# Kernel optimization log

Measured on AMD Instinct MI355X. Metric: run time of the kernel, lower is better.

The kernel has to match this reference:

```python
import jax, jax.numpy as jnp
import numpy as np

B, L, D_IN, D_H, N_CLS = 512, 256, 300, 96, 20
N = B * L            # total nodes = 131072
DEG = 8
E = N * DEG          # 1,048,576 edges
VOCAB = 50001        # num_words + 1 (padding row)
STEP = 2
NEG_SLOPE = 0.2


def setup_inputs() -> dict:
    key = jax.random.key(0)
    ks = jax.random.split(key, 24)
    node_ids = jax.random.randint(ks[0], (N,), 0, 50000)
    # block-local edges: each edge stays within its graph's node range
    gid = jnp.repeat(jnp.arange(B), L * DEG)           # [E]
    src = gid * L + jax.random.randint(ks[1], (E,), 0, L)
    dst = gid * L + jax.random.randint(ks[2], (E,), 0, L)

    def xavier(k, shape):
        fan_in, fan_out = shape[0], shape[-1]
        a = float(np.sqrt(6.0 / (fan_in + fan_out)))
        return jax.random.uniform(k, shape, jnp.float32, -a, a)

    inp = {
        "node_ids": node_ids, "src": src, "dst": dst,
        "embed": jax.random.normal(ks[3], (VOCAB, D_IN), jnp.float32),
        "We": xavier(ks[4], (D_IN, D_H)), "be": jnp.zeros((D_H,), jnp.float32),
        "Wg": xavier(ks[5], (D_H, D_H)),
        "att_src": xavier(ks[6], (D_H,)), "att_dst": xavier(ks[7], (D_H,)),
        "bg": jnp.zeros((D_H,), jnp.float32),
        "Wz0": xavier(ks[8], (D_H, D_H)), "bz0": jnp.zeros((D_H,), jnp.float32),
        "Wz1": xavier(ks[9], (D_H, D_H)), "bz1": jnp.zeros((D_H,), jnp.float32),
        "Wr0": xavier(ks[10], (D_H, D_H)), "br0": jnp.zeros((D_H,), jnp.float32),
        "Wr1": xavier(ks[11], (D_H, D_H)), "br1": jnp.zeros((D_H,), jnp.float32),
        "Wh0": xavier(ks[12], (D_H, D_H)), "bh0": jnp.zeros((D_H,), jnp.float32),
        "Wh1": xavier(ks[13], (D_H, D_H)), "bh1": jnp.zeros((D_H,), jnp.float32),
        "Wemb": xavier(ks[14], (D_H, D_H)),
        "Wmlp": xavier(ks[15], (D_H, N_CLS)),
    }
    return inp


def _forward(node_ids, src, dst, embed, We, be, Wg, att_src, att_dst, bg,
             Wz0, bz0, Wz1, bz1, Wr0, br0, Wr1, br1, Wh0, bh0, Wh1, bh1,
             Wemb, Wmlp):
    # embedding lookup + encode (dropout off, eval)
    x = embed[node_ids]                                  # [N, D_IN]
    x = jnp.tanh(x @ We + be)                            # [N, D_H]

    # self loops (GATConv add_self_loops=True, heads=1)
    loop = jnp.arange(N)
    s = jnp.concatenate([src, loop])
    d = jnp.concatenate([dst, loop])

    for _ in range(STEP):
        # ---- GATConv ----
        h = x @ Wg                                       # [N, D_H]
        a_s = h @ att_src                                # [N]
        a_d = h @ att_dst                                # [N]
        e = a_s[s] + a_d[d]
        e = jnp.where(e > 0, e, NEG_SLOPE * e)           # leaky_relu
        # segment softmax over incoming edges of each target node
        m = jax.ops.segment_max(e, d, num_segments=N)
        ex = jnp.exp(e - m[d])
        denom = jax.ops.segment_sum(ex, d, num_segments=N)
        alpha = ex / denom[d]                            # [E+N]
        a = jax.ops.segment_sum(alpha[:, None] * h[s], d, num_segments=N) + bg
        # ---- GRU update (act=tanh) ----
        z = jax.nn.sigmoid(a @ Wz0 + bz0 + x @ Wz1 + bz1)
        r = jax.nn.sigmoid(a @ Wr0 + br0 + x @ Wr1 + br1)
        hh = jnp.tanh(a @ Wh0 + bh0 + (x * r) @ Wh1 + bh1)
        x = hh * z + x * (1.0 - z)

    # graph2batch: equal-length graphs -> reshape, mask is all ones
    xb = x.reshape(B, L, D_H)
    y = jnp.tanh(xb @ Wemb)                              # [B, L, D_H]
    pooled = y.max(axis=1) + y.mean(axis=1)              # max + mean readout
    return pooled @ Wmlp                                 # [B, N_CLS]


def reference(node_ids, src, dst, embed, We, be, Wg, att_src, att_dst, bg,
              Wz0, bz0, Wz1, bz1, Wr0, br0, Wr1, br1, Wh0, bh0, Wh1, bh1,
              Wemb, Wmlp):
    return _forward(node_ids, src, dst, embed, We, be, Wg, att_src, att_dst, bg,
                    Wz0, bz0, Wz1, bz1, Wr0, br0, Wr1, br1, Wh0, bh0, Wh1, bh1,
                    Wemb, Wmlp)
```

## Files before the change

### kernel.cpp

```cpp
#include <hip/hip_runtime.h>
#include <hip/hip_bf16.h>

#define NNODES 131072
#define LGRAPH 256
#define BGRAPH 512
#define DIN 300
#define DH 96
#define EPG 2048
#define VOCAB 50001
#define NCLS 20
#define NEG 0.2f
#define EMB_ROWS 50048
#define EMB_K 320
#define WS 100
#define XS 104

typedef __attribute__((ext_vector_type(4))) float f32x4;
typedef __attribute__((ext_vector_type(8))) short bf16x8;
typedef __attribute__((ext_vector_type(8))) unsigned short u16x8;
#define MFMA16(a, b, c) __builtin_amdgcn_mfma_f32_16x16x32_bf16(a, b, c, 0, 0, 0)

__device__ __forceinline__ unsigned short f2b(float f) {
  __hip_bfloat16 h = __float2bfloat16(f);
  return *reinterpret_cast<unsigned short*>(&h);
}
__device__ __forceinline__ float b2f(unsigned short u) {
  unsigned v = ((unsigned)u) << 16;
  return __uint_as_float(v);
}
__device__ __forceinline__ float sigm(float v) { return 1.f / (1.f + __expf(-v)); }
__device__ __forceinline__ float ftanh(float x) {
  float ax = fabsf(x);
  float e = __expf(ax + ax);
  float t = 1.f - 2.f / (e + 1.f);
  return copysignf(t, x);
}

__global__ void k_prep_w(const float* __restrict__ Wg, const float* __restrict__ Wz0,
                         const float* __restrict__ Wz1, const float* __restrict__ Wr0,
                         const float* __restrict__ Wr1, const float* __restrict__ Wh0,
                         const float* __restrict__ Wh1, const float* __restrict__ Wemb,
                         const float* __restrict__ We,
                         const float* __restrict__ bz0, const float* __restrict__ bz1,
                         const float* __restrict__ br0, const float* __restrict__ br1,
                         const float* __restrict__ bh0, const float* __restrict__ bh1,
                         unsigned short* __restrict__ WT, unsigned short* __restrict__ WeT,
                         float* __restrict__ bc) {
  const int b = blockIdx.x, t = threadIdx.x;
  if (b < 8) {
    const float* src = (b == 0) ? Wg : (b == 1) ? Wz0 : (b == 2) ? Wz1 : (b == 3) ? Wr0
                     : (b == 4) ? Wr1 : (b == 5) ? Wh0 : (b == 6) ? Wh1 : Wemb;
    unsigned short* dst = WT + b * DH * DH;
    for (int i = t; i < DH * DH; i += 256) {
      int c = i / DH, k = i - c * DH;
      dst[i] = f2b(src[k * DH + c]);
    }
  } else if (b == 8) {
    for (int i = t; i < DH * EMB_K; i += 256) {
      int c = i / EMB_K, k = i - c * EMB_K;
      WeT[i] = (k < DIN) ? f2b(We[k * DH + c]) : (unsigned short)0;
    }
  } else {
    if (t < DH) {
      bc[t] = bz0[t] + bz1[t];
      bc[DH + t] = br0[t] + br1[t];
      bc[2 * DH + t] = bh0[t] + bh1[t];
    }
  }
}

__device__ __forceinline__ bf16x8 ldcvt(const float* __restrict__ p, int row, int ko) {
  bf16x8 r;
  if (row < VOCAB) {
    float4 c0 = (ko + 4 <= DIN) ? *(const float4*)&p[row * DIN + ko]
                                : make_float4(0.f, 0.f, 0.f, 0.f);
    float4 c1 = (ko + 8 <= DIN) ? *(const float4*)&p[row * DIN + ko + 4]
                                : make_float4(0.f, 0.f, 0.f, 0.f);
    r[0] = (short)f2b(c0.x); r[1] = (short)f2b(c0.y);
    r[2] = (short)f2b(c0.z); r[3] = (short)f2b(c0.w);
    r[4] = (short)f2b(c1.x); r[5] = (short)f2b(c1.y);
    r[6] = (short)f2b(c1.z); r[7] = (short)f2b(c1.w);
  } else {
    #pragma unroll
    for (int j = 0; j < 8; ++j) r[j] = 0;
  }
  return r;
}

__global__ void k_emb_mm(const float* __restrict__ embed,
                         const unsigned short* __restrict__ WeT,
                         unsigned short* __restrict__ Tb) {
  const int t = threadIdx.x, w = t >> 6, l = t & 63, li = l & 15, lh = l >> 4;
  const int wbase = blockIdx.x * 128 + w * 32;
  f32x4 acc[2][6];
  #pragma unroll
  for (int rt = 0; rt < 2; rt++)
    #pragma unroll
    for (int ct = 0; ct < 6; ct++) acc[rt][ct] = (f32x4)0.f;
  for (int ks = 0; ks < 10; ++ks) {
    const int ko = lh * 8 + ks * 32;
    bf16x8 aA0 = ldcvt(embed, wbase + li, ko);
    bf16x8 aA1 = ldcvt(embed, wbase + 16 + li, ko);
    #pragma unroll
    for (int ct = 0; ct < 6; ct++) {
      bf16x8 bB = *(const bf16x8*)&WeT[(ct * 16 + li) * EMB_K + ko];
      acc[0][ct] = MFMA16(aA0, bB, acc[0][ct]);
      acc[1][ct] = MFMA16(aA1, bB, acc[1][ct]);
    }
  }
  #pragma unroll
  for (int rt = 0; rt < 2; rt++)
    #pragma unroll
    for (int ct = 0; ct < 6; ct++)
      #pragma unroll
      for (int r = 0; r < 4; r++)
        Tb[(wbase + rt * 16 + lh * 4 + r) * DH + ct * 16 + li] = f2b(acc[rt][ct][r]);
}

__global__ void k_gather(const int* __restrict__ ids, const unsigned short* __restrict__ Tb,
                         const float* __restrict__ be, unsigned short* __restrict__ xb) {
  const int total = NNODES * (DH / 8);
  for (int i = blockIdx.x * blockDim.x + threadIdx.x; i < total;
       i += gridDim.x * blockDim.x) {
    int n = i / (DH / 8);
    int q = i - n * (DH / 8);
    u16x8 v = *(const u16x8*)&Tb[ids[n] * DH + q * 8];
    u16x8 o;
    #pragma unroll
    for (int j = 0; j < 8; ++j) o[j] = f2b(ftanh(b2f(v[j]) + be[q * 8 + j]));
    *(u16x8*)&xb[i * 8] = o;
  }
}

__global__ __launch_bounds__(256) void k_h(
    const unsigned short* __restrict__ xb, const unsigned short* __restrict__ WgT,
    const float* __restrict__ att_s, const float* __restrict__ att_d,
    unsigned short* __restrict__ h, float* __restrict__ a_s,
    float* __restrict__ a_d) {
  __shared__ __align__(16) unsigned short sW[DH * WS];
  const int t = threadIdx.x, w = t >> 6, l = t & 63, li = l & 15, lh = l >> 4;
  const int wbase = blockIdx.x * 128 + w * 32;
  for (int i = t; i < DH * 12; i += 256) {
    int r = i / 12, c8 = i - r * 12;
    *(int4*)&sW[r * WS + c8 * 8] = *(const int4*)&WgT[r * DH + c8 * 8];
  }
  __syncthreads();
  f32x4 acc[2][6];
  #pragma unroll
  for (int rt = 0; rt < 2; rt++)
    #pragma unroll
    for (int ct = 0; ct < 6; ct++) acc[rt][ct] = (f32x4)0.f;
  #pragma unroll
  for (int ks = 0; ks < 3; ++ks) {
    const int ko = lh * 8 + ks * 32;
    bf16x8 aA0 = *(const bf16x8*)&xb[(wbase + li) * DH + ko];
    bf16x8 aA1 = *(const bf16x8*)&xb[(wbase + 16 + li) * DH + ko];
    #pragma unroll
    for (int ct = 0; ct < 6; ct++) {
      bf16x8 bB = *(const bf16x8*)&sW[(ct * 16 + li) * WS + ko];
      acc[0][ct] = MFMA16(aA0, bB, acc[0][ct]);
      acc[1][ct] = MFMA16(aA1, bB, acc[1][ct]);
    }
  }
  float ps[2][4] = {}, pd[2][4] = {};
  #pragma unroll
  for (int rt = 0; rt < 2; rt++)
    #pragma unroll
    for (int ct = 0; ct < 6; ct++) {
      const int col = ct * 16 + li;
      const float as_ = att_s[col], ad_ = att_d[col];
      #pragma unroll
      for (int r = 0; r < 4; r++) {
        float v = acc[rt][ct][r];
        h[(wbase + rt * 16 + lh * 4 + r) * DH + col] = f2b(v);
        ps[rt][r] += v * as_;
        pd[rt][r] += v * ad_;
      }
    }
  #pragma unroll
  for (int rt = 0; rt < 2; rt++)
    #pragma unroll
    for (int r = 0; r < 4; r++) {
      float s = ps[rt][r], d = pd[rt][r];
      #pragma unroll
      for (int m = 1; m < 16; m <<= 1) { s += __shfl_xor(s, m); d += __shfl_xor(d, m); }
      if (li == 0) {
        const int row = wbase + rt * 16 + lh * 4 + r;
        a_s[row] = s;
        a_d[row] = d;
      }
    }
}

__global__ __launch_bounds__(512, 4) void k_att(
    const int* __restrict__ src, const int* __restrict__ dst,
    const unsigned short* __restrict__ h, const float* __restrict__ a_sg,
    const float* __restrict__ a_dg, const float* __restrict__ bg,
    unsigned short* __restrict__ aout) {
  __shared__ __align__(16) unsigned short sH[LGRAPH * XS];
  __shared__ float s_ev[EPG];
  __shared__ unsigned char s_sl[EPG], s_dl[EPG];
  __shared__ unsigned char s_srcS[EPG];
  __shared__ int s_cnt[LGRAPH], s_off[LGRAPH], s_pos[LGRAPH];
  __shared__ float s_as[LGRAPH], s_ad[LGRAPH];
  __shared__ float s_bg[DH];
  const int g = blockIdx.x, t = threadIdx.x;
  const int nb = g * LGRAPH;
  if (t < LGRAPH) { s_cnt[t] = 0; s_as[t] = a_sg[nb + t]; s_ad[t] = a_dg[nb + t]; }
  if (t < DH) s_bg[t] = bg[t];
  #pragma unroll
  for (int j = 0; j < 6; ++j) {
    int idx = t + 512 * j;
    int row = idx / 12, ch = idx - row * 12;
    *(int4*)&sH[row * XS + ch * 8] = *(const int4*)&h[(nb + row) * DH + ch * 8];
  }
  __syncthreads();
  for (int e = t; e < EPG; e += 512) {
    int sl = src[g * EPG + e] - nb, dl = dst[g * EPG + e] - nb;
    s_sl[e] = (unsigned char)sl;
    s_dl[e] = (unsigned char)dl;
    atomicAdd(&s_cnt[dl], 1);
  }
  __syncthreads();
  if (t < 64) {
    int carry = 0;
    #pragma unroll
    for (int c = 0; c < 4; ++c) {
      int v = s_cnt[c * 64 + t];
      int x = v;
      #pragma unroll
      for (int o = 1; o < 64; o <<= 1) {
        int y = __shfl_up(x, o);
        if (t >= o) x += y;
      }
      s_off[c * 64 + t] = x - v + carry;
      carry += __shfl(x, 63);
    }
  }
  __syncthreads();
  if (t < LGRAPH) s_pos[t] = s_off[t];
  __syncthreads();
  for (int e = t; e < EPG; e += 512) {
    int sl = s_sl[e], dl = s_dl[e];
    float ee = s_as[sl] + s_ad[dl];
    ee = ee > 0.f ? ee : NEG * ee;
    int pos = atomicAdd(&s_pos[dl], 1);
    s_srcS[pos] = (unsigned char)sl;
    s_ev[pos] = ee;
  }
  __syncthreads();
  {
    const int d = t >> 1, half = t & 1;
    const int beg = s_off[d], end = beg + s_cnt[d];
    float ss = s_as[d] + s_ad[d];
    ss = ss > 0.f ? ss : NEG * ss;
    float m = ss;
    for (int i = beg; i < end; ++i) m = fmaxf(m, s_ev[i]);
    const int cbase = half * 48;
    float acc[48];
    float wself = __expf(ss - m);
    float den = wself;
    #pragma unroll
    for (int k = 0; k < 6; ++k) {
      u16x8 v = *(const u16x8*)&sH[d * XS + cbase + k * 8];
      #pragma unroll
      for (int j = 0; j < 8; ++j) acc[k * 8 + j] = wself * b2f(v[j]);
    }
    for (int i = beg; i < end; ++i) {
      float wv = __expf(s_ev[i] - m);
      den += wv;
      int sl2 = s_srcS[i];
      #pragma unroll
      for (int k = 0; k < 6; ++k) {
        u16x8 v = *(const u16x8*)&sH[sl2 * XS + cbase + k * 8];
        #pragma unroll
        for (int j = 0; j < 8; ++j) acc[k * 8 + j] += wv * b2f(v[j]);
      }
    }
    float inv = 1.f / den;
    unsigned short* op = &aout[(nb + d) * DH + cbase];
    #pragma unroll
    for (int k = 0; k < 6; ++k) {
      u16x8 o;
      #pragma unroll
      for (int j = 0; j < 8; ++j) o[j] = f2b(acc[k * 8 + j] * inv + s_bg[cbase + k * 8 + j]);
      *(u16x8*)&op[k * 8] = o;
    }
  }
}

__global__ __launch_bounds__(512, 2) void k_gru(
    const unsigned short* __restrict__ ab, unsigned short* __restrict__ xb,
    const unsigned short* __restrict__ WT, const float* __restrict__ bc) {
  __shared__ __align__(16) unsigned short sW[6 * DH * WS];
  __shared__ __align__(16) unsigned short sX[128 * WS];
  const int t = threadIdx.x, w = t >> 6, l = t & 63, li = l & 15, lh = l >> 4;
  const int wr = w >> 1, wc = w & 1;
  #pragma unroll
  for (int m = 0; m < 6; ++m) {
    const int srcm = (m == 0) ? 3 : (m == 1) ? 4 : (m == 2) ? 1 : (m == 3) ? 2 : (m == 4) ? 5 : 6;
    const unsigned short* srcp = WT + srcm * DH * DH;
    for (int i = t; i < DH * 12; i += 512) {
      int r = i / 12, c8 = i - r * 12;
      *(int4*)&sW[(m * DH + r) * WS + c8 * 8] = *(const int4*)&srcp[r * DH + c8 * 8];
    }
  }
  float zb_[3], rb_[3], hb_[3];
  #pragma unroll
  for (int ct = 0; ct < 3; ++ct) {
    const int col = wc * 48 + ct * 16 + li;
    zb_[ct] = bc[col]; rb_[ct] = bc[DH + col]; hb_[ct] = bc[2 * DH + col];
  }

  for (int tile = 0; tile < 4; ++tile) {
    const int nb0 = (blockIdx.x * 4 + tile) * 128;
    __syncthreads();
    #pragma unroll
    for (int j = 0; j < 3; ++j) {
      int idx = t + 512 * j;
      int row = idx / 12, ch = idx - row * 12;
      *(int4*)&sX[row * WS + ch * 8] = *(const int4*)&xb[(nb0 + row) * DH + ch * 8];
    }
    __syncthreads();
    bf16x8 aA[2][3], aX[2][3];
    #pragma unroll
    for (int rt = 0; rt < 2; rt++)
      #pragma unroll
      for (int ks = 0; ks < 3; ks++) {
        const int row = wr * 32 + rt * 16 + li;
        const int ko = lh * 8 + ks * 32;
        aA[rt][ks] = *(const bf16x8*)&ab[(nb0 + row) * DH + ko];
        aX[rt][ks] = *(const bf16x8*)&sX[row * WS + ko];
      }
    float xo[2][3][4];
    #pragma unroll
    for (int rt = 0; rt < 2; rt++)
      #pragma unroll
      for (int ct = 0; ct < 3; ct++)
        #pragma unroll
        for (int r = 0; r < 4; r++)
          xo[rt][ct][r] = b2f(sX[(wr * 32 + rt * 16 + lh * 4 + r) * WS + wc * 48 + ct * 16 + li]);
    f32x4 accR[2][3], accZ[2][3];
    #pragma unroll
    for (int rt = 0; rt < 2; rt++)
      #pragma unroll
      for (int ct = 0; ct < 3; ct++) { accR[rt][ct] = (f32x4)0.f; accZ[rt][ct] = (f32x4)0.f; }
    #pragma unroll
    for (int ks = 0; ks < 3; ks++) {
      const int ko = lh * 8 + ks * 32;
      #pragma unroll
      for (int ct = 0; ct < 3; ct++) {
        const int wrow = wc * 48 + ct * 16 + li;
        bf16x8 w_r0 = *(const bf16x8*)&sW[(0 * DH + wrow) * WS + ko];
        bf16x8 w_r1 = *(const bf16x8*)&sW[(1 * DH + wrow) * WS + ko];
        bf16x8 w_z0 = *(const bf16x8*)&sW[(2 * DH + wrow) * WS + ko];
        bf16x8 w_z1 = *(const bf16x8*)&sW[(3 * DH + wrow) * WS + ko];
        #pragma unroll
        for (int rt = 0; rt < 2; rt++) {
          accR[rt][ct] = MFMA16(aA[rt][ks], w_r0, accR[rt][ct]);
          accR[rt][ct] = MFMA16(aX[rt][ks], w_r1, accR[rt][ct]);
          accZ[rt][ct] = MFMA16(aA[rt][ks], w_z0, accZ[rt][ct]);
          accZ[rt][ct] = MFMA16(aX[rt][ks], w_z1, accZ[rt][ct]);
        }
      }
    }
    __syncthreads();
    #pragma unroll
    for (int rt = 0; rt < 2; rt++)
      #pragma unroll
      for (int ct = 0; ct < 3; ct++) {
        const int col = wc * 48 + ct * 16 + li;
        #pragma unroll
        for (int r = 0; r < 4; r++) {
          float rv = sigm(accR[rt][ct][r] + rb_[ct]);
          sX[(wr * 32 + rt * 16 + lh * 4 + r) * WS + col] = f2b(xo[rt][ct][r] * rv);
        }
      }
    __syncthreads();
    bf16x8 aU[2][3];
    #pragma unroll
    for (int rt = 0; rt < 2; rt++)
      #pragma unroll
      for (int ks = 0; ks < 3; ks++)
        aU[rt][ks] = *(const bf16x8*)&sX[(wr * 32 + rt * 16 + li) * WS + lh * 8 + ks * 32];
    __syncthreads();
    f32x4 accH[2][3];
    #pragma unroll
    for (int rt = 0; rt < 2; rt++)
      #pragma unroll
      for (int ct = 0; ct < 3; ct++) accH[rt][ct] = (f32x4)0.f;
    #pragma unroll
    for (int ks = 0; ks < 3; ks++) {
      const int ko = lh * 8 + ks * 32;
      #pragma unroll
      for (int ct = 0; ct < 3; ct++) {
        const int wrow = wc * 48 + ct * 16 + li;
        bf16x8 w_h0 = *(const bf16x8*)&sW[(4 * DH + wrow) * WS + ko];
        bf16x8 w_h1 = *(const bf16x8*)&sW[(5 * DH + wrow) * WS + ko];
        #pragma unroll
        for (int rt = 0; rt < 2; rt++) {
          accH[rt][ct] = MFMA16(aA[rt][ks], w_h0, accH[rt][ct]);
          accH[rt][ct] = MFMA16(aU[rt][ks], w_h1, accH[rt][ct]);
        }
      }
    }
    #pragma unroll
    for (int rt = 0; rt < 2; rt++)
      #pragma unroll
      for (int ct = 0; ct < 3; ct++) {
        const int col = wc * 48 + ct * 16 + li;
        #pragma unroll
        for (int r = 0; r < 4; r++) {
          float z = sigm(accZ[rt][ct][r] + zb_[ct]);
          float hh = ftanh(accH[rt][ct][r] + hb_[ct]);
          float xn = hh * z + xo[rt][ct][r] * (1.f - z);
          sX[(wr * 32 + rt * 16 + lh * 4 + r) * WS + col] = f2b(xn);
        }
      }
    __syncthreads();
    #pragma unroll
    for (int j = 0; j < 3; ++j) {
      int idx = t + 512 * j;
      int row = idx / 12, ch = idx - row * 12;
      *(int4*)&xb[(nb0 + row) * DH + ch * 8] = *(const int4*)&sX[row * WS + ch * 8];
    }
  }
}

__global__ __launch_bounds__(256) void k_readout(
    const unsigned short* __restrict__ xb, const unsigned short* __restrict__ WembT,
    const float* __restrict__ Wmlp, float* __restrict__ out) {
  __shared__ __align__(16) unsigned short sW[DH * WS];
  __shared__ float pmaxs[4][DH], psums[4][DH];
  __shared__ float spool[DH];
  const int g = blockIdx.x, t = threadIdx.x, w = t >> 6, l = t & 63, li = l & 15, lh = l >> 4;
  const int wbase = g * LGRAPH + w * 64;
  for (int i = t; i < DH * 12; i += 256) {
    int r = i / 12, c8 = i - r * 12;
    *(int4*)&sW[r * WS + c8 * 8] = *(const int4*)&WembT[r * DH + c8 * 8];
  }
  __syncthreads();
  f32x4 acc[4][6];
  #pragma unroll
  for (int rt = 0; rt < 4; rt++)
    #pragma unroll
    for (int ct = 0; ct < 6; ct++) acc[rt][ct] = (f32x4)0.f;
  #pragma unroll
  for (int ks = 0; ks < 3; ks++) {
    const int ko = lh * 8 + ks * 32;
    bf16x8 aA[4];
    #pragma unroll
    for (int rt = 0; rt < 4; rt++)
      aA[rt] = *(const bf16x8*)&xb[(wbase + rt * 16 + li) * DH + ko];
    #pragma unroll
    for (int ct = 0; ct < 6; ct++) {
      bf16x8 bB = *(const bf16x8*)&sW[(ct * 16 + li) * WS + ko];
      #pragma unroll
      for (int rt = 0; rt < 4; rt++) acc[rt][ct] = MFMA16(aA[rt], bB, acc[rt][ct]);
    }
  }
  float pm[6], psu[6];
  #pragma unroll
  for (int ct = 0; ct < 6; ct++) {
    float mx = -1e30f, sm = 0.f;
    #pragma unroll
    for (int rt = 0; rt < 4; rt++)
      #pragma unroll
      for (int r = 0; r < 4; r++) {
        float y = ftanh(acc[rt][ct][r]);
        mx = fmaxf(mx, y);
        sm += y;
      }
    pm[ct] = mx; psu[ct] = sm;
  }
  #pragma unroll
  for (int ct = 0; ct < 6; ct++) {
    pm[ct] = fmaxf(pm[ct], __shfl_xor(pm[ct], 16));
    psu[ct] += __shfl_xor(psu[ct], 16);
    pm[ct] = fmaxf(pm[ct], __shfl_xor(pm[ct], 32));
    psu[ct] += __shfl_xor(psu[ct], 32);
  }
  if (lh == 0) {
    #pragma unroll
    for (int ct = 0; ct < 6; ct++) {
      pmaxs[w][ct * 16 + li] = pm[ct];
      psums[w][ct * 16 + li] = psu[ct];
    }
  }
  __syncthreads();
  if (t < DH) {
    float mx = fmaxf(fmaxf(pmaxs[0][t], pmaxs[1][t]), fmaxf(pmaxs[2][t], pmaxs[3][t]));
    float sm = psums[0][t] + psums[1][t] + psums[2][t] + psums[3][t];
    spool[t] = mx + sm * (1.f / LGRAPH);
  }
  __syncthreads();
  if (t < NCLS) {
    float a = 0.f;
    for (int k = 0; k < DH; ++k) a += spool[k] * Wmlp[k * NCLS + t];
    out[g * NCLS + t] = a;
  }
}

extern "C" void kernel_launch(void* const* d_in, const int* in_sizes, int n_in,
                              void* d_out, int out_size, void* d_ws, size_t ws_size,
                              hipStream_t stream) {
  const int*   node_ids = (const int*)d_in[0];
  const int*   src      = (const int*)d_in[1];
  const int*   dst      = (const int*)d_in[2];
  const float* embed    = (const float*)d_in[3];
  const float* We   = (const float*)d_in[4];
  const float* be   = (const float*)d_in[5];
  const float* Wg   = (const float*)d_in[6];
  const float* att_src = (const float*)d_in[7];
  const float* att_dst = (const float*)d_in[8];
  const float* bg   = (const float*)d_in[9];
  const float* Wz0  = (const float*)d_in[10];
  const float* bz0  = (const float*)d_in[11];
  const float* Wz1  = (const float*)d_in[12];
  const float* bz1  = (const float*)d_in[13];
  const float* Wr0  = (const float*)d_in[14];
  const float* br0  = (const float*)d_in[15];
  const float* Wr1  = (const float*)d_in[16];
  const float* br1  = (const float*)d_in[17];
  const float* Wh0  = (const float*)d_in[18];
  const float* bh0  = (const float*)d_in[19];
  const float* Wh1  = (const float*)d_in[20];
  const float* bh1  = (const float*)d_in[21];
  const float* Wemb = (const float*)d_in[22];
  const float* Wmlp = (const float*)d_in[23];
  float* out = (float*)d_out;

  char* w_ = (char*)d_ws;
  unsigned short* xb   = (unsigned short*)(w_ + 0);
  unsigned short* ab   = (unsigned short*)(w_ + 25165824);
  unsigned short* h    = (unsigned short*)(w_ + 50331648);
  unsigned short* Tb   = (unsigned short*)(w_ + 75497472);
  float*          a_s  = (float*)(w_ + 85106688);
  float*          a_d  = (float*)(w_ + 85630976);
  unsigned short* WT   = (unsigned short*)(w_ + 86155264);
  unsigned short* WeT  = (unsigned short*)(w_ + 86302720);
  float*          bc   = (float*)(w_ + 86364160);

  unsigned short* WgT  = WT + 0 * DH * DH;
  unsigned short* WembT= WT + 7 * DH * DH;

  hipLaunchKernelGGL(k_prep_w, dim3(10), dim3(256), 0, stream,
                     Wg, Wz0, Wz1, Wr0, Wr1, Wh0, Wh1, Wemb, We,
                     bz0, bz1, br0, br1, bh0, bh1, WT, WeT, bc);
  hipLaunchKernelGGL(k_emb_mm, dim3(EMB_ROWS / 128), dim3(256), 0, stream, embed, WeT, Tb);
  hipLaunchKernelGGL(k_gather, dim3(2048), dim3(256), 0, stream, node_ids, Tb, be, xb);
  for (int s = 0; s < 2; ++s) {
    hipLaunchKernelGGL(k_h, dim3(NNODES / 128), dim3(256), 0, stream,
                       xb, WgT, att_src, att_dst, h, a_s, a_d);
    hipLaunchKernelGGL(k_att, dim3(BGRAPH), dim3(512), 0, stream,
                       src, dst, h, a_s, a_d, bg, ab);
    hipLaunchKernelGGL(k_gru, dim3(256), dim3(512), 0, stream, ab, xb, WT, bc);
  }
  hipLaunchKernelGGL(k_readout, dim3(BGRAPH), dim3(256), 0, stream, xb, WembT, Wmlp, out);
}
```

Measured before the change: 246.0 us.

## Fuse embedding gather with first GAT projection and widen GRU to 12 waves

Merges the gather/tanh encode kernel with the first-step Wg projection and attention-score computation, so the encoded rows are consumed from shared memory instead of being re-read from global memory by a separate launch. The GRU kernel is also reorganised from 8 waves (4x2) to 12 waves (4x3) per block, each covering 32 output columns instead of 48, to reduce per-thread register use and add parallelism. The fused kernel holds the Wg fragments in registers, and the larger GRU block with launch bounds of 3 blocks per CU may be limited by LDS, since each block keeps all six weight matrices in shared memory.

```diff
diff --git a/kernel.cpp b/kernel.cpp
--- a/kernel.cpp
+++ b/kernel.cpp
@@ -117,19 +117,85 @@
         Tb[(wbase + rt * 16 + lh * 4 + r) * DH + ct * 16 + li] = f2b(acc[rt][ct][r]);
 }
 
-__global__ void k_gather(const int* __restrict__ ids, const unsigned short* __restrict__ Tb,
-                         const float* __restrict__ be, unsigned short* __restrict__ xb) {
-  const int total = NNODES * (DH / 8);
-  for (int i = blockIdx.x * blockDim.x + threadIdx.x; i < total;
-       i += gridDim.x * blockDim.x) {
-    int n = i / (DH / 8);
-    int q = i - n * (DH / 8);
-    u16x8 v = *(const u16x8*)&Tb[ids[n] * DH + q * 8];
+__global__ __launch_bounds__(256) void k_gh(
+    const int* __restrict__ ids, const unsigned short* __restrict__ Tb,
+    const float* __restrict__ be, const unsigned short* __restrict__ WgT,
+    const float* __restrict__ att_s, const float* __restrict__ att_d,
+    unsigned short* __restrict__ xb, unsigned short* __restrict__ h,
+    float* __restrict__ a_s, float* __restrict__ a_d) {
+  __shared__ __align__(16) unsigned short sX[128 * XS];
+  __shared__ int s_id[128];
+  __shared__ float s_be[DH];
+  const int t = threadIdx.x, w = t >> 6, l = t & 63, li = l & 15, lh = l >> 4;
+  const int nb0 = blockIdx.x * 128;
+  bf16x8 WF[6][3];
+  #pragma unroll
+  for (int ct = 0; ct < 6; ++ct)
+    #pragma unroll
+    for (int ks = 0; ks < 3; ++ks)
+      WF[ct][ks] = *(const bf16x8*)&WgT[(ct * 16 + li) * DH + lh * 8 + ks * 32];
+  if (t < 128) s_id[t] = ids[nb0 + t];
+  if (t < DH) s_be[t] = be[t];
+  __syncthreads();
+  #pragma unroll
+  for (int j = 0; j < 6; ++j) {
+    int idx = t + 256 * j;
+    int row = idx / 12, ch = idx - row * 12;
+    u16x8 v = *(const u16x8*)&Tb[s_id[row] * DH + ch * 8];
     u16x8 o;
     #pragma unroll
-    for (int j = 0; j < 8; ++j) o[j] = f2b(ftanh(b2f(v[j]) + be[q * 8 + j]));
-    *(u16x8*)&xb[i * 8] = o;
-  }
+    for (int k = 0; k < 8; ++k) o[k] = f2b(ftanh(b2f(v[k]) + s_be[ch * 8 + k]));
+    *(u16x8*)&sX[row * XS + ch * 8] = o;
+    *(u16x8*)&xb[(nb0 + row) * DH + ch * 8] = o;
+  }
+  __syncthreads();
+  const int wbase = w * 32;
+  f32x4 acc[2][6];
+  #pragma unroll
+  for (int rt = 0; rt < 2; rt++)
+    #pragma unroll
+    for (int ct = 0; ct < 6; ct++) acc[rt][ct] = (f32x4)0.f;
+  bf16x8 aA[2][3];
+  #pragma unroll
+  for (int rt = 0; rt < 2; rt++)
+    #pragma unroll
+    for (int ks = 0; ks < 3; ks++)
+      aA[rt][ks] = *(const bf16x8*)&sX[(wbase + rt * 16 + li) * XS + lh * 8 + ks * 32];
+  #pragma unroll
+  for (int ks = 0; ks < 3; ++ks)
+    #pragma unroll
+    for (int ct = 0; ct < 6; ct++) {
+      acc[0][ct] = MFMA16(aA[0][ks], WF[ct][ks], acc[0][ct]);
+      acc[1][ct] = MFMA16(aA[1][ks], WF[ct][ks], acc[1][ct]);
+    }
+  float ps[2][4] = {}, pd[2][4] = {};
+  #pragma unroll
+  for (int rt = 0; rt < 2; rt++)
+    #pragma unroll
+    for (int ct = 0; ct < 6; ct++) {
+      const int col = ct * 16 + li;
+      const float as_ = att_s[col], ad_ = att_d[col];
+      #pragma unroll
+      for (int r = 0; r < 4; r++) {
+        float v = acc[rt][ct][r];
+        h[(nb0 + wbase + rt * 16 + lh * 4 + r) * DH + col] = f2b(v);
+        ps[rt][r] += v * as_;
+        pd[rt][r] += v * ad_;
+      }
+    }
+  #pragma unroll
+  for (int rt = 0; rt < 2; rt++)
+    #pragma unroll
+    for (int r = 0; r < 4; r++) {
+      float s = ps[rt][r], d = pd[rt][r];
+      #pragma unroll
+      for (int m = 1; m < 16; m <<= 1) { s += __shfl_xor(s, m); d += __shfl_xor(d, m); }
+      if (li == 0) {
+        const int row = nb0 + wbase + rt * 16 + lh * 4 + r;
+        a_s[row] = s;
+        a_d[row] = d;
+      }
+    }
 }
 
 __global__ __launch_bounds__(256) void k_h(
@@ -289,26 +355,26 @@
   }
 }
 
-__global__ __launch_bounds__(512, 2) void k_gru(
+__global__ __launch_bounds__(768, 3) void k_gru(
     const unsigned short* __restrict__ ab, unsigned short* __restrict__ xb,
     const unsigned short* __restrict__ WT, const float* __restrict__ bc) {
   __shared__ __align__(16) unsigned short sW[6 * DH * WS];
   __shared__ __align__(16) unsigned short sX[128 * WS];
   const int t = threadIdx.x, w = t >> 6, l = t & 63, li = l & 15, lh = l >> 4;
-  const int wr = w >> 1, wc = w & 1;
+  const int wr = w / 3, wc = w - wr * 3;
   #pragma unroll
   for (int m = 0; m < 6; ++m) {
     const int srcm = (m == 0) ? 3 : (m == 1) ? 4 : (m == 2) ? 1 : (m == 3) ? 2 : (m == 4) ? 5 : 6;
     const unsigned short* srcp = WT + srcm * DH * DH;
-    for (int i = t; i < DH * 12; i += 512) {
+    for (int i = t; i < DH * 12; i += 768) {
       int r = i / 12, c8 = i - r * 12;
       *(int4*)&sW[(m * DH + r) * WS + c8 * 8] = *(const int4*)&srcp[r * DH + c8 * 8];
     }
   }
-  float zb_[3], rb_[3], hb_[3];
-  #pragma unroll
-  for (int ct = 0; ct < 3; ++ct) {
-    const int col = wc * 48 + ct * 16 + li;
+  float zb_[2], rb_[2], hb_[2];
+  #pragma unroll
+  for (int ct = 0; ct < 2; ++ct) {
+    const int col = wc * 32 + ct * 16 + li;
     zb_[ct] = bc[col]; rb_[ct] = bc[DH + col]; hb_[ct] = bc[2 * DH + col];
   }
 
@@ -316,8 +382,8 @@
     const int nb0 = (blockIdx.x * 4 + tile) * 128;
     __syncthreads();
     #pragma unroll
-    for (int j = 0; j < 3; ++j) {
-      int idx = t + 512 * j;
+    for (int j = 0; j < 2; ++j) {
+      int idx = t + 768 * j;
       int row = idx / 12, ch = idx - row * 12;
       *(int4*)&sX[row * WS + ch * 8] = *(const int4*)&xb[(nb0 + row) * DH + ch * 8];
     }
@@ -332,25 +398,25 @@
         aA[rt][ks] = *(const bf16x8*)&ab[(nb0 + row) * DH + ko];
         aX[rt][ks] = *(const bf16x8*)&sX[row * WS + ko];
       }
-    float xo[2][3][4];
+    float xo[2][2][4];
     #pragma unroll
     for (int rt = 0; rt < 2; rt++)
       #pragma unroll
-      for (int ct = 0; ct < 3; ct++)
+      for (int ct = 0; ct < 2; ct++)
         #pragma unroll
         for (int r = 0; r < 4; r++)
-          xo[rt][ct][r] = b2f(sX[(wr * 32 + rt * 16 + lh * 4 + r) * WS + wc * 48 + ct * 16 + li]);
-    f32x4 accR[2][3], accZ[2][3];
+          xo[rt][ct][r] = b2f(sX[(wr * 32 + rt * 16 + lh * 4 + r) * WS + wc * 32 + ct * 16 + li]);
+    f32x4 accR[2][2], accZ[2][2];
     #pragma unroll
     for (int rt = 0; rt < 2; rt++)
       #pragma unroll
-      for (int ct = 0; ct < 3; ct++) { accR[rt][ct] = (f32x4)0.f; accZ[rt][ct] = (f32x4)0.f; }
+      for (int ct = 0; ct < 2; ct++) { accR[rt][ct] = (f32x4)0.f; accZ[rt][ct] = (f32x4)0.f; }
     #pragma unroll
     for (int ks = 0; ks < 3; ks++) {
       const int ko = lh * 8 + ks * 32;
       #pragma unroll
-      for (int ct = 0; ct < 3; ct++) {
-        const int wrow = wc * 48 + ct * 16 + li;
+      for (int ct = 0; ct < 2; ct++) {
+        const int wrow = wc * 32 + ct * 16 + li;
         bf16x8 w_r0 = *(const bf16x8*)&sW[(0 * DH + wrow) * WS + ko];
         bf16x8 w_r1 = *(const bf16x8*)&sW[(1 * DH + wrow) * WS + ko];
         bf16x8 w_z0 = *(const bf16x8*)&sW[(2 * DH + wrow) * WS + ko];
@@ -368,8 +434,8 @@
     #pragma unroll
     for (int rt = 0; rt < 2; rt++)
       #pragma unroll
-      for (int ct = 0; ct < 3; ct++) {
-        const int col = wc * 48 + ct * 16 + li;
+      for (int ct = 0; ct < 2; ct++) {
+        const int col = wc * 32 + ct * 16 + li;
         #pragma unroll
         for (int r = 0; r < 4; r++) {
           float rv = sigm(accR[rt][ct][r] + rb_[ct]);
@@ -384,17 +450,17 @@
       for (int ks = 0; ks < 3; ks++)
         aU[rt][ks] = *(const bf16x8*)&sX[(wr * 32 + rt * 16 + li) * WS + lh * 8 + ks * 32];
     __syncthreads();
-    f32x4 accH[2][3];
+    f32x4 accH[2][2];
     #pragma unroll
     for (int rt = 0; rt < 2; rt++)
       #pragma unroll
-      for (int ct = 0; ct < 3; ct++) accH[rt][ct] = (f32x4)0.f;
+      for (int ct = 0; ct < 2; ct++) accH[rt][ct] = (f32x4)0.f;
     #pragma unroll
     for (int ks = 0; ks < 3; ks++) {
       const int ko = lh * 8 + ks * 32;
       #pragma unroll
-      for (int ct = 0; ct < 3; ct++) {
-        const int wrow = wc * 48 + ct * 16 + li;
+      for (int ct = 0; ct < 2; ct++) {
+        const int wrow = wc * 32 + ct * 16 + li;
         bf16x8 w_h0 = *(const bf16x8*)&sW[(4 * DH + wrow) * WS + ko];
         bf16x8 w_h1 = *(const bf16x8*)&sW[(5 * DH + wrow) * WS + ko];
         #pragma unroll
@@ -407,8 +473,8 @@
     #pragma unroll
     for (int rt = 0; rt < 2; rt++)
       #pragma unroll
-      for (int ct = 0; ct < 3; ct++) {
-        const int col = wc * 48 + ct * 16 + li;
+      for (int ct = 0; ct < 2; ct++) {
+        const int col = wc * 32 + ct * 16 + li;
         #pragma unroll
         for (int r = 0; r < 4; r++) {
           float z = sigm(accZ[rt][ct][r] + zb_[ct]);
@@ -419,8 +485,8 @@
       }
     __syncthreads();
     #pragma unroll
-    for (int j = 0; j < 3; ++j) {
-      int idx = t + 512 * j;
+    for (int j = 0; j < 2; ++j) {
+      int idx = t + 768 * j;
       int row = idx / 12, ch = idx - row * 12;
       *(int4*)&xb[(nb0 + row) * DH + ch * 8] = *(const int4*)&sX[row * WS + ch * 8];
     }
@@ -541,20 +607,22 @@
   unsigned short* WeT  = (unsigned short*)(w_ + 86302720);
   float*          bc   = (float*)(w_ + 86364160);
 
-  unsigned short* WgT  = WT + 0 * DH * DH;
-  unsigned short* WembT= WT + 7 * DH * DH;
+  unsigned short* WgT   = WT + 0 * DH * DH;
+  unsigned short* WembT = WT + 7 * DH * DH;
 
   hipLaunchKernelGGL(k_prep_w, dim3(10), dim3(256), 0, stream,
                      Wg, Wz0, Wz1, Wr0, Wr1, Wh0, Wh1, Wemb, We,
                      bz0, bz1, br0, br1, bh0, bh1, WT, WeT, bc);
   hipLaunchKernelGGL(k_emb_mm, dim3(EMB_ROWS / 128), dim3(256), 0, stream, embed, WeT, Tb);
-  hipLaunchKernelGGL(k_gather, dim3(2048), dim3(256), 0, stream, node_ids, Tb, be, xb);
-  for (int s = 0; s < 2; ++s) {
-    hipLaunchKernelGGL(k_h, dim3(NNODES / 128), dim3(256), 0, stream,
-                       xb, WgT, att_src, att_dst, h, a_s, a_d);
-    hipLaunchKernelGGL(k_att, dim3(BGRAPH), dim3(512), 0, stream,
-                       src, dst, h, a_s, a_d, bg, ab);
-    hipLaunchKernelGGL(k_gru, dim3(256), dim3(512), 0, stream, ab, xb, WT, bc);
-  }
+  hipLaunchKernelGGL(k_gh, dim3(NNODES / 128), dim3(256), 0, stream,
+                     node_ids, Tb, be, WgT, att_src, att_dst, xb, h, a_s, a_d);
+  hipLaunchKernelGGL(k_att, dim3(BGRAPH), dim3(512), 0, stream,
+                     src, dst, h, a_s, a_d, bg, ab);
+  hipLaunchKernelGGL(k_gru, dim3(256), dim3(768), 0, stream, ab, xb, WT, bc);
+  hipLaunchKernelGGL(k_h, dim3(NNODES / 128), dim3(256), 0, stream,
+                     xb, WgT, att_src, att_dst, h, a_s, a_d);
+  hipLaunchKernelGGL(k_att, dim3(BGRAPH), dim3(512), 0, stream,
+                     src, dst, h, a_s, a_d, bg, ab);
+  hipLaunchKernelGGL(k_gru, dim3(256), dim3(768), 0, stream, ab, xb, WT, bc);
   hipLaunchKernelGGL(k_readout, dim3(BGRAPH), dim3(256), 0, stream, xb, WembT, Wmlp, out);
 }
```

Measured after the change: 236.2 us. 1.04x faster.
